# Optimization experiments

Hardware: AMD Instinct MI355X
Metric: run time of the kernel (lower is better)

## Reference

```python
import jax, jax.numpy as jnp
import numpy as np

B, H, W = 8, 512, 512
K = 3            # kernel_size
PAD = (K - 1) // 2
K2 = K * K       # 9 taps


def setup_inputs() -> dict:
    key = jax.random.key(0)
    k1, k2, k3 = jax.random.split(key, 3)
    depth = jax.random.normal(k1, (B, 1, H, W), dtype=jnp.float32)
    weight = jax.random.uniform(k2, (B, K2, H, W), dtype=jnp.float32)      # per-pixel modulation mask
    offset = jax.random.normal(k3, (B, 2 * K2, H, W), dtype=jnp.float32)   # interleaved (dy, dx) per tap
    return {"depth": depth, "weight": weight, "offset": offset}


def _bilinear_gather(img, py, px):
    # img: [B, H, W]; py, px: [B, K2, H, W] sampling coords (zero outside boundaries)
    Bv, Hv, Wv = img.shape
    y0 = jnp.floor(py)
    x0 = jnp.floor(px)
    ty = py - y0
    tx = px - x0
    y0i = y0.astype(jnp.int32)
    x0i = x0.astype(jnp.int32)
    img_flat = img.reshape(Bv, -1)

    def corner(yi, xi, w):
        valid = (yi >= 0) & (yi < Hv) & (xi >= 0) & (xi < Wv)
        yc = jnp.clip(yi, 0, Hv - 1)
        xc = jnp.clip(xi, 0, Wv - 1)
        idx = (yc * Wv + xc).reshape(Bv, -1)
        vals = jnp.take_along_axis(img_flat, idx, axis=1).reshape(yi.shape)
        return jnp.where(valid, vals, 0.0) * w

    return (corner(y0i, x0i, (1.0 - ty) * (1.0 - tx))
            + corner(y0i, x0i + 1, (1.0 - ty) * tx)
            + corner(y0i + 1, x0i, ty * (1.0 - tx))
            + corner(y0i + 1, x0i + 1, ty * tx))


def reference(depth, weight, offset):
    # dkn_residual=True path: subtract per-pixel mean over the 9 taps
    w = weight - jnp.mean(weight, axis=1, keepdims=True)            # [B, 9, H, W]
    dy = offset[:, 0::2]                                             # [B, 9, H, W]
    dx = offset[:, 1::2]
    ky, kx = jnp.meshgrid(jnp.arange(K), jnp.arange(K), indexing="ij")
    ky = ky.reshape(-1).astype(jnp.float32)                          # [9]
    kx = kx.reshape(-1).astype(jnp.float32)
    gy = jnp.arange(H, dtype=jnp.float32)
    gx = jnp.arange(W, dtype=jnp.float32)
    # sampling coords: output pos - pad + tap offset + learned offset
    py = dy + gy[None, None, :, None] - PAD + ky[None, :, None, None]
    px = dx + gx[None, None, None, :] - PAD + kx[None, :, None, None]
    sampled = _bilinear_gather(depth[:, 0], py, px)                  # [B, 9, H, W]
    # dcn.weight == ones, dcn.bias == zeros -> mask-weighted sum over taps
    out = jnp.sum(sampled * w, axis=1, keepdims=True)                # [B, 1, H, W]
    return out + depth                                               # residual
```

## Files before the change

kernel.cpp:

```cpp
#include <hip/hip_runtime.h>

#define BB 8
#define HH 512
#define WW 512
#define K2 9
#define HW (HH * WW)

#define TX 64
#define TY 16
#define NROWS (TY + 11)
#define NCOLS (TX + 11)
#define STRIDE 77
#define NSTAGE 8

__device__ __noinline__ float gsample(const float* __restrict__ dimg,
                                      float py, float px) {
    const float y0f = floorf(py);
    const float x0f = floorf(px);
    const float ty = py - y0f;
    const float tx = px - x0f;
    const int y0 = (int)y0f, x0 = (int)x0f;
    const int y1 = y0 + 1,   x1 = x0 + 1;
    const int y0c = min(max(y0, 0), HH - 1);
    const int y1c = min(max(y1, 0), HH - 1);
    const int x0c = min(max(x0, 0), WW - 1);
    const int x1c = min(max(x1, 0), WW - 1);
    const float v00 = dimg[y0c * WW + x0c];
    const float v01 = dimg[y0c * WW + x1c];
    const float v10 = dimg[y1c * WW + x0c];
    const float v11 = dimg[y1c * WW + x1c];
    const bool vy0 = (unsigned)y0 < HH, vy1 = (unsigned)y1 < HH;
    const bool vx0 = (unsigned)x0 < WW, vx1 = (unsigned)x1 < WW;
    const float w00 = (vy0 & vx0) ? (1.f - ty) * (1.f - tx) : 0.f;
    const float w01 = (vy0 & vx1) ? (1.f - ty) * tx         : 0.f;
    const float w10 = (vy1 & vx0) ? ty * (1.f - tx)         : 0.f;
    const float w11 = (vy1 & vx1) ? ty * tx                 : 0.f;
    return v00 * w00 + v01 * w01 + v10 * w10 + v11 * w11;
}

struct B3 { float4 w0, w1, w2, dy0, dy1, dy2, dx0, dx1, dx2; };

template<int KB>
__device__ __forceinline__ void load_b3(B3& r,
                                        const float* __restrict__ wp,
                                        const float* __restrict__ op) {
    r.dy0 = *(const float4*)(op + (2 * (KB + 0)    ) * HW);
    r.dx0 = *(const float4*)(op + (2 * (KB + 0) + 1) * HW);
    r.dy1 = *(const float4*)(op + (2 * (KB + 1)    ) * HW);
    r.dx1 = *(const float4*)(op + (2 * (KB + 1) + 1) * HW);
    r.dy2 = *(const float4*)(op + (2 * (KB + 2)    ) * HW);
    r.dx2 = *(const float4*)(op + (2 * (KB + 2) + 1) * HW);
    r.w0  = *(const float4*)(wp + (KB + 0) * HW);
    r.w1  = *(const float4*)(wp + (KB + 1) * HW);
    r.w2  = *(const float4*)(wp + (KB + 2) * HW);
}

#define SAMPLE(dyv, dxv, xoff, sj)                                          \
    do {                                                                    \
        const float py = (dyv) + ybase;                                     \
        const float px = (dxv) + xbase + (float)(xoff);                     \
        const float y0f = floorf(py);                                       \
        const float x0f = floorf(px);                                       \
        const float fty = py - y0f;                                         \
        const float ftx = px - x0f;                                         \
        const int iy = (int)y0f - ry0;                                      \
        const int ix = (int)x0f - cx0;                                      \
        if ((unsigned)iy < NROWS - 1 && (unsigned)ix < NCOLS - 1) {         \
            const float* q = tile + iy * STRIDE + ix;                       \
            const float v00 = q[0], v01 = q[1];                             \
            const float v10 = q[STRIDE], v11 = q[STRIDE + 1];               \
            const float a0 = v00 + ftx * (v01 - v00);                       \
            const float a1 = v10 + ftx * (v11 - v10);                       \
            sj = a0 + fty * (a1 - a0);                                      \
        } else {                                                            \
            sj = gsample(dimg, py, px);                                     \
        }                                                                   \
    } while (0)

#define DO_K(K, w4, dy4, dx4)                                               \
    do {                                                                    \
        const float ybase = (float)(y - 1 + (K) / 3);                       \
        const float xbase = (float)(x - 1 + (K) % 3);                       \
        float s0, s1, s2, s3;                                               \
        SAMPLE((dy4).x, (dx4).x, 0, s0);                                    \
        SAMPLE((dy4).y, (dx4).y, 1, s1);                                    \
        SAMPLE((dy4).z, (dx4).z, 2, s2);                                    \
        SAMPLE((dy4).w, (dx4).w, 3, s3);                                    \
        accw.x += s0 * (w4).x;  accs.x += s0;  wsum.x += (w4).x;            \
        accw.y += s1 * (w4).y;  accs.y += s1;  wsum.y += (w4).y;            \
        accw.z += s2 * (w4).z;  accs.z += s2;  wsum.z += (w4).z;            \
        accw.w += s3 * (w4).w;  accs.w += s3;  wsum.w += (w4).w;            \
    } while (0)

__global__ __launch_bounds__(256, 4) void pp_deconv_kernel(
    const float* __restrict__ depth,
    const float* __restrict__ weight,
    const float* __restrict__ offset,
    float* __restrict__ out)
{
    __shared__ float tile[NROWS * STRIDE];

    const int tid = threadIdx.x;
    const int tx0 = blockIdx.x * TX;
    const int ty0 = blockIdx.y * TY;
    const int b   = blockIdx.z;

    const int ry0 = ty0 - 5;
    const int cx0 = tx0 - 5;

    const float* dimg = depth + (size_t)b * HW;

    float sv[NSTAGE];
    int   sa[NSTAGE];
#pragma unroll
    for (int u = 0; u < NSTAGE; ++u) {
        const int li = tid + u * 256;
        float v = 0.f;
        int   a = -1;
        if (li < NROWS * NCOLS) {
            const int r  = li / NCOLS;
            const int c  = li - r * NCOLS;
            const int gy = ry0 + r;
            const int gx = cx0 + c;
            if ((unsigned)gy < HH && (unsigned)gx < WW) v = dimg[gy * WW + gx];
            a = r * STRIDE + c;
        }
        sv[u] = v;
        sa[u] = a;
    }

    const int xl = (tid & 15) << 2;
    const int yl = tid >> 4;
    const int x = tx0 + xl;
    const int y = ty0 + yl;
    const int p = y * WW + x;

    const float* wp = weight + (size_t)b * K2 * HW + p;
    const float* op = offset + (size_t)b * 2 * K2 * HW + p;

    B3 A, Bq;
    load_b3<0>(A, wp, op);
    load_b3<3>(Bq, wp, op);

#pragma unroll
    for (int u = 0; u < NSTAGE; ++u)
        if (sa[u] >= 0) tile[sa[u]] = sv[u];
    __syncthreads();

    float4 accw = make_float4(0.f, 0.f, 0.f, 0.f);
    float4 accs = make_float4(0.f, 0.f, 0.f, 0.f);
    float4 wsum = make_float4(0.f, 0.f, 0.f, 0.f);

    DO_K(0, A.w0, A.dy0, A.dx0);
    DO_K(1, A.w1, A.dy1, A.dx1);
    DO_K(2, A.w2, A.dy2, A.dx2);

    B3 C;
    load_b3<6>(C, wp, op);

    DO_K(3, Bq.w0, Bq.dy0, Bq.dx0);
    DO_K(4, Bq.w1, Bq.dy1, Bq.dx1);
    DO_K(5, Bq.w2, Bq.dy2, Bq.dx2);

    DO_K(6, C.w0, C.dy0, C.dx0);
    DO_K(7, C.w1, C.dy1, C.dx1);
    DO_K(8, C.w2, C.dy2, C.dx2);

    const float* dq = tile + (yl + 5) * STRIDE + (xl + 5);
    const float c9 = 1.0f / 9.0f;
    float4 o;
    o.x = accw.x - wsum.x * c9 * accs.x + dq[0];
    o.y = accw.y - wsum.y * c9 * accs.y + dq[1];
    o.z = accw.z - wsum.z * c9 * accs.z + dq[2];
    o.w = accw.w - wsum.w * c9 * accs.w + dq[3];
    *(float4*)(out + (size_t)b * HW + p) = o;
}

extern "C" void kernel_launch(void* const* d_in, const int* in_sizes, int n_in,
                              void* d_out, int out_size, void* d_ws, size_t ws_size,
                              hipStream_t stream) {
    const float* depth  = (const float*)d_in[0];
    const float* weight = (const float*)d_in[1];
    const float* offset = (const float*)d_in[2];
    float* out = (float*)d_out;

    dim3 grid(WW / TX, HH / TY, BB);
    dim3 block(256);
    pp_deconv_kernel<<<grid, block, 0, stream>>>(depth, weight, offset, out);
}
```

Measured before the change: 277.1 us.

## Make tile sampling branchless with deferred out-of-tile correction and hoist all loads

Every tap now reads the shared-memory tile at clamped coordinates without branching and sets a bit in a 36-bit mask when the sample fell outside the tile. A rare fix-up pass then reloads those taps from global memory and adds the difference between the true sample and the clamped one. All 27 offset/weight float4 loads are issued at once behind scheduling barriers, the tile staging writes go to a padding slot instead of being guarded, and the occupancy hint drops from 4 to 3 waves to fit the extra registers. The aim is to remove divergent branches and expose more memory parallelism, at the cost of higher register pressure and lower occupancy.

Measured after the change: 278.9 us. No clear change (+0.7%).

```diff
diff --git a/kernel.cpp b/kernel.cpp
--- a/kernel.cpp
+++ b/kernel.cpp
@@ -12,9 +12,12 @@
 #define NCOLS (TX + 11)
 #define STRIDE 77
 #define NSTAGE 8
-
-__device__ __noinline__ float gsample(const float* __restrict__ dimg,
-                                      float py, float px) {
+#define TILE_PAD (NROWS * STRIDE)
+
+#define SFENCE() __builtin_amdgcn_sched_barrier(0)
+
+__device__ __forceinline__ float gsample(const float* __restrict__ dimg,
+                                         float py, float px) {
     const float y0f = floorf(py);
     const float x0f = floorf(px);
     const float ty = py - y0f;
@@ -38,24 +41,7 @@
     return v00 * w00 + v01 * w01 + v10 * w10 + v11 * w11;
 }
 
-struct B3 { float4 w0, w1, w2, dy0, dy1, dy2, dx0, dx1, dx2; };
-
-template<int KB>
-__device__ __forceinline__ void load_b3(B3& r,
-                                        const float* __restrict__ wp,
-                                        const float* __restrict__ op) {
-    r.dy0 = *(const float4*)(op + (2 * (KB + 0)    ) * HW);
-    r.dx0 = *(const float4*)(op + (2 * (KB + 0) + 1) * HW);
-    r.dy1 = *(const float4*)(op + (2 * (KB + 1)    ) * HW);
-    r.dx1 = *(const float4*)(op + (2 * (KB + 1) + 1) * HW);
-    r.dy2 = *(const float4*)(op + (2 * (KB + 2)    ) * HW);
-    r.dx2 = *(const float4*)(op + (2 * (KB + 2) + 1) * HW);
-    r.w0  = *(const float4*)(wp + (KB + 0) * HW);
-    r.w1  = *(const float4*)(wp + (KB + 1) * HW);
-    r.w2  = *(const float4*)(wp + (KB + 2) * HW);
-}
-
-#define SAMPLE(dyv, dxv, xoff, sj)                                          \
+#define SAMPLE_BL(dyv, dxv, xoff, sj, KK, JJ)                               \
     do {                                                                    \
         const float py = (dyv) + ybase;                                     \
         const float px = (dxv) + xbase + (float)(xoff);                     \
@@ -65,40 +51,41 @@
         const float ftx = px - x0f;                                         \
         const int iy = (int)y0f - ry0;                                      \
         const int ix = (int)x0f - cx0;                                      \
-        if ((unsigned)iy < NROWS - 1 && (unsigned)ix < NCOLS - 1) {         \
-            const float* q = tile + iy * STRIDE + ix;                       \
-            const float v00 = q[0], v01 = q[1];                             \
-            const float v10 = q[STRIDE], v11 = q[STRIDE + 1];               \
-            const float a0 = v00 + ftx * (v01 - v00);                       \
-            const float a1 = v10 + ftx * (v11 - v10);                       \
-            sj = a0 + fty * (a1 - a0);                                      \
-        } else {                                                            \
-            sj = gsample(dimg, py, px);                                     \
-        }                                                                   \
+        const int iyc = min(max(iy, 0), NROWS - 2);                         \
+        const int ixc = min(max(ix, 0), NCOLS - 2);                         \
+        bad |= (unsigned long long)                                         \
+               (((unsigned)iy >= NROWS - 1) | ((unsigned)ix >= NCOLS - 1))  \
+               << ((KK) * 4 + (JJ));                                        \
+        const float* q = tile + iyc * STRIDE + ixc;                         \
+        const float v00 = q[0], v01 = q[1];                                 \
+        const float v10 = q[STRIDE], v11 = q[STRIDE + 1];                   \
+        const float a0 = v00 + ftx * (v01 - v00);                           \
+        const float a1 = v10 + ftx * (v11 - v10);                           \
+        sj = a0 + fty * (a1 - a0);                                          \
     } while (0)
 
-#define DO_K(K, w4, dy4, dx4)                                               \
+#define DO_K(KK, w4, dy4, dx4)                                              \
     do {                                                                    \
-        const float ybase = (float)(y - 1 + (K) / 3);                       \
-        const float xbase = (float)(x - 1 + (K) % 3);                       \
+        const float ybase = (float)(y - 1 + (KK) / 3);                      \
+        const float xbase = (float)(x - 1 + (KK) % 3);                      \
         float s0, s1, s2, s3;                                               \
-        SAMPLE((dy4).x, (dx4).x, 0, s0);                                    \
-        SAMPLE((dy4).y, (dx4).y, 1, s1);                                    \
-        SAMPLE((dy4).z, (dx4).z, 2, s2);                                    \
-        SAMPLE((dy4).w, (dx4).w, 3, s3);                                    \
+        SAMPLE_BL((dy4).x, (dx4).x, 0, s0, KK, 0);                          \
+        SAMPLE_BL((dy4).y, (dx4).y, 1, s1, KK, 1);                          \
+        SAMPLE_BL((dy4).z, (dx4).z, 2, s2, KK, 2);                          \
+        SAMPLE_BL((dy4).w, (dx4).w, 3, s3, KK, 3);                          \
         accw.x += s0 * (w4).x;  accs.x += s0;  wsum.x += (w4).x;            \
         accw.y += s1 * (w4).y;  accs.y += s1;  wsum.y += (w4).y;            \
         accw.z += s2 * (w4).z;  accs.z += s2;  wsum.z += (w4).z;            \
         accw.w += s3 * (w4).w;  accs.w += s3;  wsum.w += (w4).w;            \
     } while (0)
 
-__global__ __launch_bounds__(256, 4) void pp_deconv_kernel(
+__global__ __launch_bounds__(256, 3) void pp_deconv_kernel(
     const float* __restrict__ depth,
     const float* __restrict__ weight,
     const float* __restrict__ offset,
     float* __restrict__ out)
 {
-    __shared__ float tile[NROWS * STRIDE];
+    __shared__ float tile[NROWS * STRIDE + 1];
 
     const int tid = threadIdx.x;
     const int tx0 = blockIdx.x * TX;
@@ -115,19 +102,19 @@
 #pragma unroll
     for (int u = 0; u < NSTAGE; ++u) {
         const int li = tid + u * 256;
+        const int r  = li / NCOLS;
+        const int c  = li - r * NCOLS;
+        const int gy = ry0 + r;
+        const int gx = cx0 + c;
         float v = 0.f;
-        int   a = -1;
-        if (li < NROWS * NCOLS) {
-            const int r  = li / NCOLS;
-            const int c  = li - r * NCOLS;
-            const int gy = ry0 + r;
-            const int gx = cx0 + c;
-            if ((unsigned)gy < HH && (unsigned)gx < WW) v = dimg[gy * WW + gx];
-            a = r * STRIDE + c;
-        }
+        if ((unsigned)gy < HH && (unsigned)gx < WW) v = dimg[gy * WW + gx];
         sv[u] = v;
-        sa[u] = a;
+        sa[u] = (li < NROWS * NCOLS) ? (r * STRIDE + c) : TILE_PAD;
     }
+    SFENCE();
+#pragma unroll
+    for (int u = 0; u < NSTAGE; ++u) tile[sa[u]] = sv[u];
+    __syncthreads();
 
     const int xl = (tid & 15) << 2;
     const int yl = tid >> 4;
@@ -138,33 +125,81 @@
     const float* wp = weight + (size_t)b * K2 * HW + p;
     const float* op = offset + (size_t)b * 2 * K2 * HW + p;
 
-    B3 A, Bq;
-    load_b3<0>(A, wp, op);
-    load_b3<3>(Bq, wp, op);
-
-#pragma unroll
-    for (int u = 0; u < NSTAGE; ++u)
-        if (sa[u] >= 0) tile[sa[u]] = sv[u];
-    __syncthreads();
+    const float4 dy0 = *(const float4*)(op +  0 * HW);
+    const float4 dx0 = *(const float4*)(op +  1 * HW);
+    const float4 w0  = *(const float4*)(wp +  0 * HW);
+    const float4 dy1 = *(const float4*)(op +  2 * HW);
+    const float4 dx1 = *(const float4*)(op +  3 * HW);
+    const float4 w1  = *(const float4*)(wp +  1 * HW);
+    const float4 dy2 = *(const float4*)(op +  4 * HW);
+    const float4 dx2 = *(const float4*)(op +  5 * HW);
+    const float4 w2  = *(const float4*)(wp +  2 * HW);
+    const float4 dy3 = *(const float4*)(op +  6 * HW);
+    const float4 dx3 = *(const float4*)(op +  7 * HW);
+    const float4 w3  = *(const float4*)(wp +  3 * HW);
+    const float4 dy4 = *(const float4*)(op +  8 * HW);
+    const float4 dx4 = *(const float4*)(op +  9 * HW);
+    const float4 w4  = *(const float4*)(wp +  4 * HW);
+    const float4 dy5 = *(const float4*)(op + 10 * HW);
+    const float4 dx5 = *(const float4*)(op + 11 * HW);
+    const float4 w5  = *(const float4*)(wp +  5 * HW);
+    const float4 dy6 = *(const float4*)(op + 12 * HW);
+    const float4 dx6 = *(const float4*)(op + 13 * HW);
+    const float4 w6  = *(const float4*)(wp +  6 * HW);
+    const float4 dy7 = *(const float4*)(op + 14 * HW);
+    const float4 dx7 = *(const float4*)(op + 15 * HW);
+    const float4 w7  = *(const float4*)(wp +  7 * HW);
+    const float4 dy8 = *(const float4*)(op + 16 * HW);
+    const float4 dx8 = *(const float4*)(op + 17 * HW);
+    const float4 w8  = *(const float4*)(wp +  8 * HW);
+    SFENCE();
 
     float4 accw = make_float4(0.f, 0.f, 0.f, 0.f);
     float4 accs = make_float4(0.f, 0.f, 0.f, 0.f);
     float4 wsum = make_float4(0.f, 0.f, 0.f, 0.f);
-
-    DO_K(0, A.w0, A.dy0, A.dx0);
-    DO_K(1, A.w1, A.dy1, A.dx1);
-    DO_K(2, A.w2, A.dy2, A.dx2);
-
-    B3 C;
-    load_b3<6>(C, wp, op);
-
-    DO_K(3, Bq.w0, Bq.dy0, Bq.dx0);
-    DO_K(4, Bq.w1, Bq.dy1, Bq.dx1);
-    DO_K(5, Bq.w2, Bq.dy2, Bq.dx2);
-
-    DO_K(6, C.w0, C.dy0, C.dx0);
-    DO_K(7, C.w1, C.dy1, C.dx1);
-    DO_K(8, C.w2, C.dy2, C.dx2);
+    unsigned long long bad = 0ULL;
+
+    DO_K(0, w0, dy0, dx0);
+    DO_K(1, w1, dy1, dx1);
+    DO_K(2, w2, dy2, dx2);
+    DO_K(3, w3, dy3, dx3);
+    DO_K(4, w4, dy4, dx4);
+    DO_K(5, w5, dy5, dx5);
+    DO_K(6, w6, dy6, dx6);
+    DO_K(7, w7, dy7, dx7);
+    DO_K(8, w8, dy8, dx8);
+
+    if (__builtin_expect(bad != 0ULL, 0)) {
+#pragma unroll
+        for (int j = 0; j < 4; ++j) {
+            if (!((bad >> j) & 0x111111111ULL)) continue;
+#pragma unroll 1
+            for (int k = 0; k < K2; ++k) {
+                if (!((bad >> (k * 4 + j)) & 1ULL)) continue;
+                const float dyv = op[(2 * k) * HW + j];
+                const float dxv = op[(2 * k + 1) * HW + j];
+                const float wv  = wp[k * HW + j];
+                const float ybase = (float)(y - 1 + k / 3);
+                const float xbase = (float)(x - 1 + k % 3);
+                const float py = dyv + ybase;
+                const float px = dxv + xbase + (float)j;
+                const float y0f = floorf(py), x0f = floorf(px);
+                const float fty = py - y0f,  ftx = px - x0f;
+                const int iy = (int)y0f - ry0, ix = (int)x0f - cx0;
+                const int iyc = min(max(iy, 0), NROWS - 2);
+                const int ixc = min(max(ix, 0), NCOLS - 2);
+                const float* q = tile + iyc * STRIDE + ixc;
+                const float a0 = q[0] + ftx * (q[1] - q[0]);
+                const float a1 = q[STRIDE] + ftx * (q[STRIDE + 1] - q[STRIDE]);
+                const float wrong = a0 + fty * (a1 - a0);
+                const float d = gsample(dimg, py, px) - wrong;
+                if (j == 0) { accw.x += d * wv; accs.x += d; }
+                if (j == 1) { accw.y += d * wv; accs.y += d; }
+                if (j == 2) { accw.z += d * wv; accs.z += d; }
+                if (j == 3) { accw.w += d * wv; accs.w += d; }
+            }
+        }
+    }
 
     const float* dq = tile + (yl + 5) * STRIDE + (xl + 5);
     const float c9 = 1.0f / 9.0f;
```
